# Kernel optimization log

Hardware: AMD Instinct MI355X
Metric: run time of the kernel (lower is better)

## Reference

```python
import jax, jax.numpy as jnp
import numpy as np

H, W = 256, 256
TANFOV = 0.5
FX = W / (2.0 * TANFOV)
FY = H / (2.0 * TANFOV)
SH_C0 = 0.28209479177387814


def quat_to_rot(q):
    # q: [P,4] (r,x,y,z), assumed normalized
    r, x, y, z = q[:, 0], q[:, 1], q[:, 2], q[:, 3]
    return jnp.stack([
        jnp.stack([1 - 2 * (y * y + z * z), 2 * (x * y - r * z), 2 * (x * z + r * y)], -1),
        jnp.stack([2 * (x * y + r * z), 1 - 2 * (x * x + z * z), 2 * (y * z - r * x)], -1),
        jnp.stack([2 * (x * z - r * y), 2 * (y * z + r * x), 1 - 2 * (x * x + y * y)], -1),
    ], -2)  # [P,3,3]


def setup_inputs() -> dict:
    key = jax.random.key(0)
    ks = jax.random.split(key, 5)
    P = 512
    points = jax.random.normal(ks[0], (P, 3), jnp.float32) * 1.5
    scales = jax.random.normal(ks[1], (P, 3), jnp.float32) * 0.3 - 2.5
    rots = jax.random.normal(ks[2], (P, 4), jnp.float32)
    opacities = jax.random.normal(ks[3], (P, 1), jnp.float32)
    shs = jax.random.normal(ks[4], (P, 1, 3), jnp.float32)
    # world-to-camera: identity rotation, camera 6 units back so cloud sits at z~6
    viewmat = jnp.eye(4, dtype=jnp.float32).at[2, 3].set(6.0)
    return {"points": points, "scales": scales, "rots": rots,
            "opacities": opacities, "shs": shs, "viewmat": viewmat}


def reference(points, scales, rots, opacities, shs, viewmat):
    P = points.shape[0]
    # --- activations (as in GausRast.forward) ---
    s = jnp.exp(scales)                                   # [P,3]
    opac = jax.nn.sigmoid(opacities)[:, 0]                # [P]
    q = rots / jnp.linalg.norm(rots, axis=-1, keepdims=True)
    # --- 3D covariance: Sigma = R S S^T R^T ---
    R = quat_to_rot(q)
    M = R * s[:, None, :]                                 # R @ diag(s)
    Sigma = M @ jnp.swapaxes(M, 1, 2)                     # [P,3,3]
    # --- view transform ---
    Wrot = viewmat[:3, :3]
    t = points @ Wrot.T + viewmat[:3, 3]                  # [P,3] camera space
    tz = t[:, 2]
    visible = tz > 0.2
    tz_s = jnp.where(visible, tz, 1.0)                    # safe z
    lim = 1.3 * TANFOV
    txtz = jnp.clip(t[:, 0] / tz_s, -lim, lim) * tz_s
    tytz = jnp.clip(t[:, 1] / tz_s, -lim, lim) * tz_s
    zeros = jnp.zeros_like(tz_s)
    # EWA Jacobian [P,2,3]
    J = jnp.stack([
        jnp.stack([FX / tz_s, zeros, -FX * txtz / (tz_s * tz_s)], -1),
        jnp.stack([zeros, FY / tz_s, -FY * tytz / (tz_s * tz_s)], -1)], -2)
    Tm = jnp.einsum('pij,jk->pik', J, Wrot)               # [P,2,3]
    cov = Tm @ Sigma @ jnp.swapaxes(Tm, 1, 2)             # [P,2,2]
    det_orig = cov[:, 0, 0] * cov[:, 1, 1] - cov[:, 0, 1] ** 2
    # low-pass filter (+0.3 I) with antialiasing opacity compensation
    a = cov[:, 0, 0] + 0.3
    c = cov[:, 1, 1] + 0.3
    b = cov[:, 0, 1]
    det = a * c - b * b
    visible = visible & (det > 0)
    det_s = jnp.where(det > 0, det, 1.0)
    comp = jnp.sqrt(jnp.maximum(det_orig / det_s, 0.0))
    opac_eff = opac * comp
    conA, conB, conC = c / det_s, -b / det_s, a / det_s   # conic (inverse 2x2)
    mid = 0.5 * (a + c)
    lam = mid + jnp.sqrt(jnp.maximum(mid * mid - det, 0.1))
    radii = jnp.where(visible, jnp.ceil(3.0 * jnp.sqrt(lam)), 0.0).astype(jnp.int32)
    # projected pixel-space means
    mx = FX * t[:, 0] / tz_s + (W - 1) * 0.5
    my = FY * t[:, 1] / tz_s + (H - 1) * 0.5
    # colors from degree-0 SH
    colors = jnp.maximum(shs[:, 0, :] * SH_C0 + 0.5, 0.0)  # [P,3]
    # --- depth sort (front-to-back) ---
    order = jnp.argsort(jnp.where(visible, tz, jnp.inf))
    mx, my = mx[order], my[order]
    cA, cB, cC = conA[order], conB[order], conC[order]
    op = (opac_eff * visible.astype(opac_eff.dtype))[order]
    col = colors[order]
    # --- per-pixel Gaussian weights [P,H,W] ---
    xs = jnp.arange(W, dtype=jnp.float32)
    ys = jnp.arange(H, dtype=jnp.float32)
    dx = xs[None, None, :] - mx[:, None, None]            # [P,1,W]
    dy = ys[None, :, None] - my[:, None, None]            # [P,H,1]
    power = (-0.5 * (cA[:, None, None] * dx * dx + cC[:, None, None] * dy * dy)
             - cB[:, None, None] * dx * dy)               # [P,H,W]
    alpha = (power <= 0.0) * jnp.minimum(0.99, op[:, None, None] * jnp.exp(jnp.minimum(power, 0.0)))
    alpha = alpha * (alpha >= 1.0 / 255.0)
    # --- front-to-back alpha compositing ---
    Tcum = jnp.cumprod(1.0 - alpha, axis=0)
    Texcl = jnp.concatenate([jnp.ones((1, H, W), alpha.dtype), Tcum[:-1]], axis=0)
    wgt = alpha * Texcl * (Texcl >= 1e-4)                 # early-termination mask
    rgb = jnp.einsum('phw,pc->chw', wgt, col)             # bg is black -> no bg term
    # viewspace_points in the torch module is a zeros grad-holder
    viewspace_points = jnp.zeros_like(points)
    return rgb, viewspace_points, radii
```

## Files before the change

kernel.cpp:

```cpp
#include <hip/hip_runtime.h>
#include <math.h>

#define PNUM 512
#define IMW 256
#define IMH 256
#define NCH 8
#define SEGW 64


__global__ __launch_bounds__(512) void gr_preprocess(
    const float* __restrict__ points, const float* __restrict__ scales,
    const float* __restrict__ rots, const float* __restrict__ opac_in,
    const float* __restrict__ shs, const float* __restrict__ vm,
    float* __restrict__ out, float* __restrict__ ws)
{
    __shared__ float s_key[PNUM];
    const int i = threadIdx.x;

    const float px = points[3*i], py = points[3*i+1], pz = points[3*i+2];
    const float sx = expf(scales[3*i]), sy = expf(scales[3*i+1]), sz = expf(scales[3*i+2]);
    const float op0 = 1.0f / (1.0f + expf(-opac_in[i]));
    float q0 = rots[4*i], q1 = rots[4*i+1], q2 = rots[4*i+2], q3 = rots[4*i+3];
    const float inv = 1.0f / sqrtf(q0*q0 + q1*q1 + q2*q2 + q3*q3);
    const float r = q0*inv, x = q1*inv, y = q2*inv, z = q3*inv;

    const float R00 = 1.f - 2.f*(y*y + z*z);
    const float R01 = 2.f*(x*y - r*z);
    const float R02 = 2.f*(x*z + r*y);
    const float R10 = 2.f*(x*y + r*z);
    const float R11 = 1.f - 2.f*(x*x + z*z);
    const float R12 = 2.f*(y*z - r*x);
    const float R20 = 2.f*(x*z - r*y);
    const float R21 = 2.f*(y*z + r*x);
    const float R22 = 1.f - 2.f*(x*x + y*y);

    const float M00=R00*sx, M01=R01*sy, M02=R02*sz;
    const float M10=R10*sx, M11=R11*sy, M12=R12*sz;
    const float M20=R20*sx, M21=R21*sy, M22=R22*sz;

    const float S00 = M00*M00 + M01*M01 + M02*M02;
    const float S01 = M00*M10 + M01*M11 + M02*M12;
    const float S02 = M00*M20 + M01*M21 + M02*M22;
    const float S11 = M10*M10 + M11*M11 + M12*M12;
    const float S12 = M10*M20 + M11*M21 + M12*M22;
    const float S22 = M20*M20 + M21*M21 + M22*M22;

    const float W00=vm[0], W01=vm[1], W02=vm[2],  T0=vm[3];
    const float W10=vm[4], W11=vm[5], W12=vm[6],  T1=vm[7];
    const float W20=vm[8], W21=vm[9], W22=vm[10], T2=vm[11];
    const float tx = W00*px + W01*py + W02*pz + T0;
    const float ty = W10*px + W11*py + W12*pz + T1;
    const float tz = W20*px + W21*py + W22*pz + T2;

    bool vis = tz > 0.2f;
    const float tzs = vis ? tz : 1.0f;
    const float lim = 1.3f * 0.5f;
    const float txtz = fminf(fmaxf(tx / tzs, -lim), lim) * tzs;
    const float tytz = fminf(fmaxf(ty / tzs, -lim), lim) * tzs;

    const float FX = 256.0f, FY = 256.0f;
    const float J00 = FX / tzs;
    const float J02 = -FX * txtz / (tzs * tzs);
    const float J11 = FY / tzs;
    const float J12 = -FY * tytz / (tzs * tzs);

    const float Tm00 = J00*W00 + J02*W20;
    const float Tm01 = J00*W01 + J02*W21;
    const float Tm02 = J00*W02 + J02*W22;
    const float Tm10 = J11*W10 + J12*W20;
    const float Tm11 = J11*W11 + J12*W21;
    const float Tm12 = J11*W12 + J12*W22;

    const float U00 = Tm00*S00 + Tm01*S01 + Tm02*S02;
    const float U01 = Tm00*S01 + Tm01*S11 + Tm02*S12;
    const float U02 = Tm00*S02 + Tm01*S12 + Tm02*S22;
    const float U10 = Tm10*S00 + Tm11*S01 + Tm12*S02;
    const float U11 = Tm10*S01 + Tm11*S11 + Tm12*S12;
    const float U12 = Tm10*S02 + Tm11*S12 + Tm12*S22;

    const float cov00 = U00*Tm00 + U01*Tm01 + U02*Tm02;
    const float cov01 = U00*Tm10 + U01*Tm11 + U02*Tm12;
    const float cov11 = U10*Tm10 + U11*Tm11 + U12*Tm12;

    const float det_orig = cov00*cov11 - cov01*cov01;
    const float a = cov00 + 0.3f, c = cov11 + 0.3f, b = cov01;
    const float det = a*c - b*b;
    vis = vis && (det > 0.f);
    const float dets = (det > 0.f) ? det : 1.0f;
    const float comp = sqrtf(fmaxf(det_orig / dets, 0.f));
    const float op = vis ? op0 * comp : 0.f;
    const float cA = c / dets, cB = -b / dets, cC = a / dets;

    const float mid = 0.5f * (a + c);
    const float lam = mid + sqrtf(fmaxf(mid*mid - det, 0.1f));
    const float radii = vis ? ceilf(3.f * sqrtf(lam)) : 0.f;

    const float mx = FX * tx / tzs + (IMW - 1) * 0.5f;
    const float my = FY * ty / tzs + (IMH - 1) * 0.5f;

    const float SH_C0 = 0.28209479177387814f;
    const float cr = fmaxf(shs[3*i  ] * SH_C0 + 0.5f, 0.f);
    const float cg = fmaxf(shs[3*i+1] * SH_C0 + 0.5f, 0.f);
    const float cb = fmaxf(shs[3*i+2] * SH_C0 + 0.5f, 0.f);

    float rc2 = -1.f;
    const float p255 = 255.f * op;
    if (p255 > 1.f) rc2 = 2.f * lam * logf(p255) * 1.001f + 0.01f;

    const float key = vis ? tz : __builtin_inff();
    s_key[i] = key;
    __syncthreads();

    int rank = 0;
    #pragma unroll 8
    for (int j = 0; j < PNUM; ++j) {
        const float kj = s_key[j];
        rank += (kj < key || (kj == key && j < i)) ? 1 : 0;
    }

    ws[0*PNUM + rank] = mx;
    ws[1*PNUM + rank] = my;
    ws[2*PNUM + rank] = -0.5f * cA;
    ws[3*PNUM + rank] = -cB;
    ws[4*PNUM + rank] = -0.5f * cC;
    ws[5*PNUM + rank] = op;
    ws[6*PNUM + rank] = cr;
    ws[7*PNUM + rank] = cg;
    ws[8*PNUM + rank] = cb;
    ws[9*PNUM + rank] = rc2;

    out[196608 + 3*i + 0] = 0.f;
    out[196608 + 3*i + 1] = 0.f;
    out[196608 + 3*i + 2] = 0.f;
    out[198144 + i] = radii;
}

__global__ __launch_bounds__(512) void gr_rasterize(
    const float* __restrict__ ws, float* __restrict__ out)
{
    __shared__ int slist[PNUM];
    __shared__ int scnt[NCH];
    __shared__ float pr[NCH * SEGW], pg[NCH * SEGW], pb[NCH * SEGW], pt[NCH * SEGW];

    const int tid  = threadIdx.x;
    const int lane = tid & 63;
    const int wv   = tid >> 6;
    const int seg  = blockIdx.x;
    const int row  = seg >> 2;
    const int x0   = (seg & 3) << 6;
    const float fy = (float)row;

    const float mx  = ws[0*PNUM + tid];
    const float my  = ws[1*PNUM + tid];
    const float rc2 = ws[9*PNUM + tid];
    const float dxl = (float)x0 - mx;
    const float dxr = mx - (float)(x0 + SEGW - 1);
    const float dxm = fmaxf(0.f, fmaxf(dxl, dxr));
    const float dym = fabsf(fy - my);
    const bool hit = (dxm*dxm + dym*dym) <= rc2;

    const unsigned long long m = __ballot(hit);
    if (lane == 0) scnt[wv] = __popcll(m);
    __syncthreads();
    int base = 0;
    #pragma unroll
    for (int w = 0; w < NCH; ++w) if (w < wv) base += scnt[w];
    int L = base;
    #pragma unroll
    for (int w = 0; w < NCH; ++w) if (w >= wv) L += scnt[w];
    if (hit) {
        const int pos = __popcll(m & ((1ull << lane) - 1ull));
        slist[base + pos] = tid;
    }
    __syncthreads();

    const int Lc = (L + NCH - 1) / NCH;
    const int k0 = wv * Lc;
    const int k1 = (k0 + Lc < L) ? (k0 + Lc) : L;

    const float fx = (float)(x0 + lane);
    float T = 1.f, r = 0.f, g = 0.f, b = 0.f;

    for (int k = k0; k < k1; ++k) {
        const int j = slist[k];
        const float gmx = ws[0*PNUM + j];
        const float gmy = ws[1*PNUM + j];
        const float gA  = ws[2*PNUM + j];
        const float gB  = ws[3*PNUM + j];
        const float gC  = ws[4*PNUM + j];
        const float gop = ws[5*PNUM + j];
        const float dx = fx - gmx;
        const float dy = fy - gmy;
        const float power = fmaf(gA, dx*dx, fmaf(gB, dx*dy, gC*dy*dy));
        if (power > 0.f) continue;
        const float alpha = fminf(0.99f, gop * __expf(power));
        if (alpha < (1.0f / 255.0f)) continue;
        const float w = alpha * T;
        r = fmaf(w, ws[6*PNUM + j], r);
        g = fmaf(w, ws[7*PNUM + j], g);
        b = fmaf(w, ws[8*PNUM + j], b);
        T *= (1.f - alpha);
    }

    pr[wv * SEGW + lane] = r;
    pg[wv * SEGW + lane] = g;
    pb[wv * SEGW + lane] = b;
    pt[wv * SEGW + lane] = T;
    __syncthreads();

    if (tid < SEGW) {
        float Tc = 1.f, ar = 0.f, ag = 0.f, ab = 0.f;
        #pragma unroll
        for (int c = 0; c < NCH; ++c) {
            ar = fmaf(Tc, pr[c * SEGW + tid], ar);
            ag = fmaf(Tc, pg[c * SEGW + tid], ag);
            ab = fmaf(Tc, pb[c * SEGW + tid], ab);
            Tc *= pt[c * SEGW + tid];
        }
        const int pix = row * IMW + x0 + tid;
        out[pix]          = ar;
        out[65536 + pix]  = ag;
        out[131072 + pix] = ab;
    }
}

extern "C" void kernel_launch(void* const* d_in, const int* in_sizes, int n_in,
                              void* d_out, int out_size, void* d_ws, size_t ws_size,
                              hipStream_t stream) {
    const float* points = (const float*)d_in[0];
    const float* scales = (const float*)d_in[1];
    const float* rots   = (const float*)d_in[2];
    const float* opac   = (const float*)d_in[3];
    const float* shs    = (const float*)d_in[4];
    const float* vm     = (const float*)d_in[5];
    float* out = (float*)d_out;
    float* ws  = (float*)d_ws;

    gr_preprocess<<<1, PNUM, 0, stream>>>(points, scales, rots, opac, shs, vm, out, ws);
    gr_rasterize<<<IMH * (IMW / SEGW), 512, 0, stream>>>(ws, out);
}
```

Before: 82.98 us.

## Fuse preprocessing into rasterizer and sort only per-segment hit Gaussians

Merges the single-block preprocess kernel into the rasterizer, so every block recomputes all 512 Gaussian projections itself instead of reading a workspace. Depth sorting now ranks only the Gaussians that overlap the block's segment, and their parameters are staged in shared memory ordered by rank. This removes a kernel launch, the serialized single-block preprocess with its full O(P^2) rank loop, and the global indirect loads in the hot loop. In exchange each block repeats the preprocessing math, uses more shared memory, and switches to fast exp/log intrinsics that may change precision slightly.

```diff
diff --git a/kernel.cpp b/kernel.cpp
--- a/kernel.cpp
+++ b/kernel.cpp
@@ -7,22 +7,34 @@
 #define NCH 8
 #define SEGW 64
 
-
-__global__ __launch_bounds__(512) void gr_preprocess(
+__global__ __launch_bounds__(512, 4) void gr_fused(
     const float* __restrict__ points, const float* __restrict__ scales,
     const float* __restrict__ rots, const float* __restrict__ opac_in,
     const float* __restrict__ shs, const float* __restrict__ vm,
-    float* __restrict__ out, float* __restrict__ ws)
+    float* __restrict__ out)
 {
-    __shared__ float s_key[PNUM];
-    const int i = threadIdx.x;
-
+    __shared__ float k_tz[PNUM];
+    __shared__ int   k_id[PNUM];
+    __shared__ float smx[PNUM], smy[PNUM], sA[PNUM], sB[PNUM], sC[PNUM];
+    __shared__ float sop[PNUM], scr[PNUM], scg[PNUM], scb[PNUM];
+    __shared__ float pr[NCH*SEGW], pg[NCH*SEGW], pb[NCH*SEGW], pt[NCH*SEGW];
+    __shared__ int scnt[NCH];
+
+    const int tid  = threadIdx.x;
+    const int lane = tid & 63;
+    const int wv   = tid >> 6;
+    const int seg  = blockIdx.x;
+    const int row  = seg >> 2;
+    const int x0   = (seg & 3) << 6;
+    const float fy = (float)row;
+
+    const int i = tid;
     const float px = points[3*i], py = points[3*i+1], pz = points[3*i+2];
-    const float sx = expf(scales[3*i]), sy = expf(scales[3*i+1]), sz = expf(scales[3*i+2]);
-    const float op0 = 1.0f / (1.0f + expf(-opac_in[i]));
-    float q0 = rots[4*i], q1 = rots[4*i+1], q2 = rots[4*i+2], q3 = rots[4*i+3];
-    const float inv = 1.0f / sqrtf(q0*q0 + q1*q1 + q2*q2 + q3*q3);
-    const float r = q0*inv, x = q1*inv, y = q2*inv, z = q3*inv;
+    const float sx = __expf(scales[3*i]), sy = __expf(scales[3*i+1]), sz = __expf(scales[3*i+2]);
+    const float op0 = 1.0f / (1.0f + __expf(-opac_in[i]));
+    const float q0 = rots[4*i], q1 = rots[4*i+1], q2 = rots[4*i+2], q3 = rots[4*i+3];
+    const float qinv = 1.0f / sqrtf(q0*q0 + q1*q1 + q2*q2 + q3*q3);
+    const float r = q0*qinv, x = q1*qinv, y = q2*qinv, z = q3*qinv;
 
     const float R00 = 1.f - 2.f*(y*y + z*z);
     const float R01 = 2.f*(x*y - r*z);
@@ -87,13 +99,15 @@
     const float det = a*c - b*b;
     vis = vis && (det > 0.f);
     const float dets = (det > 0.f) ? det : 1.0f;
-    const float comp = sqrtf(fmaxf(det_orig / dets, 0.f));
-    const float op = vis ? op0 * comp : 0.f;
-    const float cA = c / dets, cB = -b / dets, cC = a / dets;
+    const float compn = sqrtf(fmaxf(det_orig / dets, 0.f));
+    const float op = vis ? op0 * compn : 0.f;
+    const float invdet = 1.0f / dets;
+    const float A2 = -0.5f * c * invdet;
+    const float B2 = b * invdet;
+    const float C2 = -0.5f * a * invdet;
 
     const float mid = 0.5f * (a + c);
     const float lam = mid + sqrtf(fmaxf(mid*mid - det, 0.1f));
-    const float radii = vis ? ceilf(3.f * sqrtf(lam)) : 0.f;
 
     const float mx = FX * tx / tzs + (IMW - 1) * 0.5f;
     const float my = FY * ty / tzs + (IMH - 1) * 0.5f;
@@ -105,72 +119,44 @@
 
     float rc2 = -1.f;
     const float p255 = 255.f * op;
-    if (p255 > 1.f) rc2 = 2.f * lam * logf(p255) * 1.001f + 0.01f;
-
-    const float key = vis ? tz : __builtin_inff();
-    s_key[i] = key;
-    __syncthreads();
-
-    int rank = 0;
-    #pragma unroll 8
-    for (int j = 0; j < PNUM; ++j) {
-        const float kj = s_key[j];
-        rank += (kj < key || (kj == key && j < i)) ? 1 : 0;
-    }
-
-    ws[0*PNUM + rank] = mx;
-    ws[1*PNUM + rank] = my;
-    ws[2*PNUM + rank] = -0.5f * cA;
-    ws[3*PNUM + rank] = -cB;
-    ws[4*PNUM + rank] = -0.5f * cC;
-    ws[5*PNUM + rank] = op;
-    ws[6*PNUM + rank] = cr;
-    ws[7*PNUM + rank] = cg;
-    ws[8*PNUM + rank] = cb;
-    ws[9*PNUM + rank] = rc2;
-
-    out[196608 + 3*i + 0] = 0.f;
-    out[196608 + 3*i + 1] = 0.f;
-    out[196608 + 3*i + 2] = 0.f;
-    out[198144 + i] = radii;
-}
-
-__global__ __launch_bounds__(512) void gr_rasterize(
-    const float* __restrict__ ws, float* __restrict__ out)
-{
-    __shared__ int slist[PNUM];
-    __shared__ int scnt[NCH];
-    __shared__ float pr[NCH * SEGW], pg[NCH * SEGW], pb[NCH * SEGW], pt[NCH * SEGW];
-
-    const int tid  = threadIdx.x;
-    const int lane = tid & 63;
-    const int wv   = tid >> 6;
-    const int seg  = blockIdx.x;
-    const int row  = seg >> 2;
-    const int x0   = (seg & 3) << 6;
-    const float fy = (float)row;
-
-    const float mx  = ws[0*PNUM + tid];
-    const float my  = ws[1*PNUM + tid];
-    const float rc2 = ws[9*PNUM + tid];
+    if (p255 > 1.f) rc2 = 2.f * lam * __logf(p255) * 1.001f + 0.01f;
+
+    if (seg == 0) {
+        const float radii = vis ? ceilf(3.f * sqrtf(lam)) : 0.f;
+        out[196608 + 3*i + 0] = 0.f;
+        out[196608 + 3*i + 1] = 0.f;
+        out[196608 + 3*i + 2] = 0.f;
+        out[198144 + i] = radii;
+    }
+
     const float dxl = (float)x0 - mx;
     const float dxr = mx - (float)(x0 + SEGW - 1);
     const float dxm = fmaxf(0.f, fmaxf(dxl, dxr));
     const float dym = fabsf(fy - my);
     const bool hit = (dxm*dxm + dym*dym) <= rc2;
 
-    const unsigned long long m = __ballot(hit);
-    if (lane == 0) scnt[wv] = __popcll(m);
-    __syncthreads();
-    int base = 0;
+    const unsigned long long mball = __ballot(hit);
+    if (lane == 0) scnt[wv] = __popcll(mball);
+    __syncthreads();
+    int base = 0, L = 0;
     #pragma unroll
-    for (int w = 0; w < NCH; ++w) if (w < wv) base += scnt[w];
-    int L = base;
-    #pragma unroll
-    for (int w = 0; w < NCH; ++w) if (w >= wv) L += scnt[w];
+    for (int w = 0; w < NCH; ++w) { L += scnt[w]; if (w < wv) base += scnt[w]; }
     if (hit) {
-        const int pos = __popcll(m & ((1ull << lane) - 1ull));
-        slist[base + pos] = tid;
+        const int pos = base + __popcll(mball & ((1ull << lane) - 1ull));
+        k_tz[pos] = tz;
+        k_id[pos] = tid;
+    }
+    __syncthreads();
+
+    if (hit) {
+        int rank = 0;
+        for (int j = 0; j < L; ++j) {
+            const float kj = k_tz[j];
+            rank += (kj < tz || (kj == tz && k_id[j] < tid)) ? 1 : 0;
+        }
+        smx[rank] = mx;  smy[rank] = my;
+        sA[rank]  = A2;  sB[rank]  = B2;  sC[rank] = C2;
+        sop[rank] = op;  scr[rank] = cr;  scg[rank] = cg;  scb[rank] = cb;
     }
     __syncthreads();
 
@@ -179,48 +165,41 @@
     const int k1 = (k0 + Lc < L) ? (k0 + Lc) : L;
 
     const float fx = (float)(x0 + lane);
-    float T = 1.f, r = 0.f, g = 0.f, b = 0.f;
+    float T = 1.f, ar = 0.f, ag = 0.f, ab = 0.f;
 
     for (int k = k0; k < k1; ++k) {
-        const int j = slist[k];
-        const float gmx = ws[0*PNUM + j];
-        const float gmy = ws[1*PNUM + j];
-        const float gA  = ws[2*PNUM + j];
-        const float gB  = ws[3*PNUM + j];
-        const float gC  = ws[4*PNUM + j];
-        const float gop = ws[5*PNUM + j];
-        const float dx = fx - gmx;
-        const float dy = fy - gmy;
-        const float power = fmaf(gA, dx*dx, fmaf(gB, dx*dy, gC*dy*dy));
+        const float dx = fx - smx[k];
+        const float dy = fy - smy[k];
+        const float power = fmaf(sA[k], dx*dx, fmaf(sB[k], dx*dy, sC[k]*dy*dy));
         if (power > 0.f) continue;
-        const float alpha = fminf(0.99f, gop * __expf(power));
+        const float alpha = fminf(0.99f, sop[k] * __expf(power));
         if (alpha < (1.0f / 255.0f)) continue;
         const float w = alpha * T;
-        r = fmaf(w, ws[6*PNUM + j], r);
-        g = fmaf(w, ws[7*PNUM + j], g);
-        b = fmaf(w, ws[8*PNUM + j], b);
+        ar = fmaf(w, scr[k], ar);
+        ag = fmaf(w, scg[k], ag);
+        ab = fmaf(w, scb[k], ab);
         T *= (1.f - alpha);
     }
 
-    pr[wv * SEGW + lane] = r;
-    pg[wv * SEGW + lane] = g;
-    pb[wv * SEGW + lane] = b;
+    pr[wv * SEGW + lane] = ar;
+    pg[wv * SEGW + lane] = ag;
+    pb[wv * SEGW + lane] = ab;
     pt[wv * SEGW + lane] = T;
     __syncthreads();
 
     if (tid < SEGW) {
-        float Tc = 1.f, ar = 0.f, ag = 0.f, ab = 0.f;
+        float Tc = 1.f, rr = 0.f, gg = 0.f, bb = 0.f;
         #pragma unroll
-        for (int c = 0; c < NCH; ++c) {
-            ar = fmaf(Tc, pr[c * SEGW + tid], ar);
-            ag = fmaf(Tc, pg[c * SEGW + tid], ag);
-            ab = fmaf(Tc, pb[c * SEGW + tid], ab);
-            Tc *= pt[c * SEGW + tid];
+        for (int c2 = 0; c2 < NCH; ++c2) {
+            rr = fmaf(Tc, pr[c2 * SEGW + tid], rr);
+            gg = fmaf(Tc, pg[c2 * SEGW + tid], gg);
+            bb = fmaf(Tc, pb[c2 * SEGW + tid], bb);
+            Tc *= pt[c2 * SEGW + tid];
         }
         const int pix = row * IMW + x0 + tid;
-        out[pix]          = ar;
-        out[65536 + pix]  = ag;
-        out[131072 + pix] = ab;
+        out[pix]          = rr;
+        out[65536 + pix]  = gg;
+        out[131072 + pix] = bb;
     }
 }
 
@@ -234,8 +213,6 @@
     const float* shs    = (const float*)d_in[4];
     const float* vm     = (const float*)d_in[5];
     float* out = (float*)d_out;
-    float* ws  = (float*)d_ws;
-
-    gr_preprocess<<<1, PNUM, 0, stream>>>(points, scales, rots, opac, shs, vm, out, ws);
-    gr_rasterize<<<IMH * (IMW / SEGW), 512, 0, stream>>>(ws, out);
+
+    gr_fused<<<IMH * (IMW / SEGW), 512, 0, stream>>>(points, scales, rots, opac, shs, vm, out);
 }
```

After: 72.76 us. 12.3% less time.
